# Optimization experiments

Measured on AMD Instinct MI355X. Metric: run time of the kernel, lower is better.

The kernel has to match this reference:

```python
import jax, jax.numpy as jnp
import numpy as np

B, T, D, H = 8, 512, 1024, 16
DK = D // H  # 64
EPS = 1e-3  # Keras BatchNormalization default epsilon


def batchnorm(x, gamma, beta):
    # Keras BN over feature axis (-1), training-mode batch statistics over (B, T)
    mean = jnp.mean(x, axis=(0, 1), keepdims=True)
    var = jnp.var(x, axis=(0, 1), keepdims=True)
    return (x - mean) * jax.lax.rsqrt(var + EPS) * gamma + beta


def setup_inputs() -> dict:
    key = jax.random.key(0)
    ks = jax.random.split(key, 12)
    s = 0.05
    return {
        "x": jax.random.normal(ks[0], (B, T, D), dtype=jnp.float32),
        "Wq": jax.random.uniform(ks[1], (H, D, DK), dtype=jnp.float32, minval=-s, maxval=s),
        "Wk": jax.random.uniform(ks[2], (H, D, DK), dtype=jnp.float32, minval=-s, maxval=s),
        "Wv": jax.random.uniform(ks[3], (H, D, DK), dtype=jnp.float32, minval=-s, maxval=s),
        "W": jax.random.uniform(ks[4], (D, D), dtype=jnp.float32, minval=-s, maxval=s),
        "W1": jax.random.normal(ks[5], (D, D), dtype=jnp.float32) * 0.02,
        "b1": jnp.zeros((D,), dtype=jnp.float32),
        "W2": jax.random.normal(ks[6], (D, D), dtype=jnp.float32) * 0.02,
        "b2": jnp.zeros((D,), dtype=jnp.float32),
        "g1": jnp.ones((D,), dtype=jnp.float32),
        "be1": jnp.zeros((D,), dtype=jnp.float32),
        "g2": jnp.ones((D,), dtype=jnp.float32),
        "be2": jnp.zeros((D,), dtype=jnp.float32),
    }


def reference(x, Wq, Wk, Wv, W, W1, b1, W2, b2, g1, be1, g2, be2):
    # Batched multi-head attention (replaces the per-head Python loop)
    q = jnp.einsum("btd,hdk->bhtk", x, Wq)
    k = jnp.einsum("btd,hdk->bhtk", x, Wk)
    v = jnp.einsum("btd,hdk->bhtk", x, Wv)
    scores = jnp.einsum("bhtk,bhsk->bhts", q, k) / jnp.sqrt(jnp.float32(DK))
    w = jax.nn.softmax(scores, axis=-1)
    attn = jnp.einsum("bhts,bhsk->bhtk", w, v)
    # concat heads: [B,H,T,DK] -> [B,T,H*DK] (head-major concat order as in the loop)
    concat = jnp.transpose(attn, (0, 2, 1, 3)).reshape(B, T, D)
    out = concat @ W
    out1 = batchnorm(x + out, g1, be1)
    out2 = jax.nn.relu(out1 @ W1 + b1) @ W2 + b2
    return batchnorm(out1 + out2, g2, be2)
```

## Files before the change

kernel.cpp:

```cpp
#include <hip/hip_runtime.h>
#include <hip/hip_bf16.h>
#include <cstdint>

#define Bn 8
#define Tn 512
#define Dn 1024
#define Hn 16
#define DKn 64
#define Mn (Bn * Tn)

typedef unsigned short u16;
typedef short bf16x8 __attribute__((ext_vector_type(8)));
typedef float f32x4 __attribute__((ext_vector_type(4)));

__device__ __forceinline__ u16 f2bf(float f) {
  unsigned int u = __builtin_bit_cast(unsigned int, f);
  u += 0x7fffu + ((u >> 16) & 1u);
  return (u16)(u >> 16);
}
__device__ __forceinline__ float bf2f(u16 v) {
  return __builtin_bit_cast(float, (unsigned int)v << 16);
}
__device__ __forceinline__ unsigned int pack2bf(float lo, float hi) {
  return (unsigned int)f2bf(lo) | ((unsigned int)f2bf(hi) << 16);
}

__device__ __forceinline__ void gl2lds16(const void* g, void* l) {
  __builtin_amdgcn_global_load_lds(
      (const __attribute__((address_space(1))) unsigned int*)g,
      (__attribute__((address_space(3))) unsigned int*)l,
      16, 0, 0);
}

__device__ __forceinline__ void bar() {
  asm volatile("" ::: "memory");
  __builtin_amdgcn_s_barrier();
  asm volatile("" ::: "memory");
}
#define WAITV(n_) asm volatile("s_waitcnt vmcnt(" #n_ ")" ::: "memory")

__global__ __launch_bounds__(256) void prep_k(
    const float* __restrict__ x, u16* __restrict__ xb,
    const float* __restrict__ wq, const float* __restrict__ wk,
    const float* __restrict__ wv, u16* __restrict__ wqkvT,
    const float* __restrict__ W, const float* __restrict__ W1,
    const float* __restrict__ W2, u16* __restrict__ wt,
    u16* __restrict__ w1t, u16* __restrict__ w2t)
{
  const int bid = blockIdx.x;
  const int t = threadIdx.x;
  if (bid < 2048) {
    const size_t i = ((size_t)bid * 256 + t) * 8;
    float4 a = *reinterpret_cast<const float4*>(&x[i]);
    float4 b = *reinterpret_cast<const float4*>(&x[i + 4]);
    uint4 w;
    w.x = pack2bf(a.x, a.y); w.y = pack2bf(a.z, a.w);
    w.z = pack2bf(b.x, b.y); w.w = pack2bf(b.z, b.w);
    *reinterpret_cast<uint4*>(&xb[i]) = w;
  } else if (bid < 2816) {
    const int idx = bid - 2048;
    const int kt = idx & 15;
    const int y  = idx >> 4;
    const int tau = y >> 4, head = y & 15;
    const float* src = (tau == 0 ? wq : tau == 1 ? wk : wv) + (size_t)head * 65536;
    const int n  = t & 63;
    const int kq = (t >> 6) << 4;
    const int k0 = kt << 6;
    u16 v[16];
#pragma unroll
    for (int j = 0; j < 16; j++)
      v[j] = f2bf(src[(size_t)(k0 + kq + j) * 64 + n]);
    u16* d = &wqkvT[((size_t)tau * 1024 + head * 64 + n) * 1024 + k0 + kq];
    *reinterpret_cast<uint4*>(&d[0]) = *reinterpret_cast<uint4*>(&v[0]);
    *reinterpret_cast<uint4*>(&d[8]) = *reinterpret_cast<uint4*>(&v[8]);
  } else {
    const int idx = bid - 2816;
    const int kt = idx & 15;
    const int rest = idx >> 4;
    const int ntl = rest & 15, z = rest >> 4;
    const float* src = (z == 0 ? W : z == 1 ? W1 : W2);
    u16* dst = (z == 0 ? wt : z == 1 ? w1t : w2t);
    const int n  = (ntl << 6) + (t & 63);
    const int kq = (t >> 6) << 4;
    const int k0 = kt << 6;
    u16 v[16];
#pragma unroll
    for (int j = 0; j < 16; j++)
      v[j] = f2bf(src[(size_t)(k0 + kq + j) * 1024 + n]);
    u16* d = &dst[(size_t)n * 1024 + k0 + kq];
    *reinterpret_cast<uint4*>(&d[0]) = *reinterpret_cast<uint4*>(&v[0]);
    *reinterpret_cast<uint4*>(&d[8]) = *reinterpret_cast<uint4*>(&v[8]);
  }
}

template<int VT>
__global__ __launch_bounds__(512) void mgemm_k(
    const u16* __restrict__ A, const u16* __restrict__ Bt,
    u16* __restrict__ Cb, int ldc, u16* __restrict__ Vt)
{
  __shared__ __align__(16) u16 As[3][4096];
  __shared__ __align__(16) u16 Bs[3][4096];

  const int nwg = gridDim.x * gridDim.y;
  const int fid = blockIdx.y * gridDim.x + blockIdx.x;
  const int lid = (fid & 7) * (nwg >> 3) + (fid >> 3);
  const int bx = lid % gridDim.x, by = lid / gridDim.x;

  const int tid  = threadIdx.x;
  const int lane = tid & 63;
  const int wid  = tid >> 6;
  const int wm = wid >> 2, wn = wid & 3;
  const int g4 = lane >> 4, r15 = lane & 15;
  const int m0 = by << 7, n0 = bx << 7;

  const int srow  = tid >> 2;
  const int sslot = tid & 3;
  const int ssw   = (srow ^ (srow >> 2)) & 3;
  const int sk8   = ((sslot ^ ssw) << 3);
  const u16* ga0 = &A[(size_t)(m0 + srow) * 1024 + sk8];
  const u16* gb0 = &Bt[(size_t)(n0 + srow) * 1024 + sk8];
  const int lofs = wid * 1024;

  f32x4 acc[4][2] = {};

  auto stage_t = [&](int t, int buf) {
    gl2lds16(ga0 + t * 32, (char*)As[buf] + lofs);
    gl2lds16(gb0 + t * 32, (char*)Bs[buf] + lofs);
  };
  auto compute_t = [&](int buf) {
    bf16x8 af[4], bfr[2];
#pragma unroll
    for (int m = 0; m < 4; m++) {
      int row = wm * 64 + m * 16 + r15;
      int sw = (row ^ (row >> 2)) & 3;
      af[m] = *reinterpret_cast<const bf16x8*>(
          (const char*)As[buf] + row * 64 + ((g4 ^ sw) << 4));
    }
#pragma unroll
    for (int n = 0; n < 2; n++) {
      int row = wn * 32 + n * 16 + r15;
      int sw = (row ^ (row >> 2)) & 3;
      bfr[n] = *reinterpret_cast<const bf16x8*>(
          (const char*)Bs[buf] + row * 64 + ((g4 ^ sw) << 4));
    }
#pragma unroll
    for (int m = 0; m < 4; m++)
#pragma unroll
      for (int n = 0; n < 2; n++)
        acc[m][n] = __builtin_amdgcn_mfma_f32_16x16x32_bf16(af[m], bfr[n], acc[m][n], 0, 0, 0);
  };

  stage_t(0, 0);
  stage_t(1, 1);

  int rd = 0, wr = 2;
#pragma unroll 1
  for (int t = 0; t < 30; ++t) {
    stage_t(t + 2, wr);
    WAITV(4);
    bar();
    compute_t(rd);
    bar();
    wr = rd;
    rd = (rd + 1 == 3) ? 0 : rd + 1;
  }
  WAITV(2);
  bar();
  compute_t(0);
  bar();
  WAITV(0);
  bar();
  compute_t(1);

  if (VT && bx >= 16) {
    const int vcol0 = n0 - 2048;
#pragma unroll
    for (int m = 0; m < 4; m++) {
      int row0 = m0 + wm * 64 + m * 16 + g4 * 4;
      int bI = row0 >> 9, s = row0 & 511;
#pragma unroll
      for (int n = 0; n < 2; n++) {
        int cv = vcol0 + wn * 32 + n * 16 + r15;
        int hh = cv >> 6, dk = cv & 63;
        uint2 pk;
        pk.x = pack2bf(acc[m][n][0], acc[m][n][1]);
        pk.y = pack2bf(acc[m][n][2], acc[m][n][3]);
        *reinterpret_cast<uint2*>(
            &Vt[(((size_t)(bI * 16 + hh) * 64 + dk) << 9) + s]) = pk;
      }
    }
    return;
  }

#pragma unroll
  for (int m = 0; m < 4; m++) {
    int row = m0 + wm * 64 + m * 16 + g4 * 4;
#pragma unroll
    for (int n = 0; n < 2; n++) {
      int col = n0 + wn * 32 + n * 16 + r15;
#pragma unroll
      for (int j = 0; j < 4; j++)
        Cb[(size_t)(row + j) * ldc + col] = f2bf(acc[m][n][j]);
    }
  }
}

template<int BIAS, int RELU, int OUTM, int RES, int RESNORM>
__global__ __launch_bounds__(512) void mgemm64_k(
    const u16* __restrict__ A, const u16* __restrict__ Bt,
    const float* __restrict__ bias, u16* __restrict__ Cb,
    const float* __restrict__ RresF, const u16* __restrict__ RresB,
    u16* __restrict__ Rout,
    float* __restrict__ psum, float* __restrict__ psumsq,
    const float* __restrict__ nsc, const float* __restrict__ nsh)
{
  __shared__ __align__(16) u16 As[3][2048];
  __shared__ __align__(16) u16 Bs[3][4096];

  const int nwg = gridDim.x * gridDim.y;
  const int fid = blockIdx.y * gridDim.x + blockIdx.x;
  const int lid = (fid & 7) * (nwg >> 3) + (fid >> 3);
  const int bx = lid % gridDim.x, by = lid / gridDim.x;

  const int tid  = threadIdx.x;
  const int lane = tid & 63;
  const int wid  = tid >> 6;
  const int wm = wid >> 2, wn = wid & 3;
  const int g4 = lane >> 4, r15 = lane & 15;
  const int m0 = by << 6, n0 = bx << 7;

  const int srow  = lane >> 2;
  const int sslot = lane & 3;
  const int arow  = (wid & 3) * 16 + srow;
  const int asw   = (arow ^ (arow >> 2)) & 3;
  const u16* gaP  = &A[(size_t)(m0 + arow) * 1024 + ((sslot ^ asw) << 3)];
  const int brow  = wid * 16 + srow;
  const int bsw   = (brow ^ (brow >> 2)) & 3;
  const u16* gbP  = &Bt[(size_t)(n0 + brow) * 1024 + ((sslot ^ bsw) << 3)];

  f32x4 acc[2][2] = {};

  auto stage_t = [&](int t, int buf) {
    if (wid < 4)
      gl2lds16(gaP + t * 32, (char*)As[buf] + (wid & 3) * 1024);
    gl2lds16(gbP + t * 32, (char*)Bs[buf] + wid * 1024);
  };
  auto compute_t = [&](int buf) {
    bf16x8 af[2], bfr[2];
#pragma unroll
    for (int m = 0; m < 2; m++) {
      int row = wm * 32 + m * 16 + r15;
      int sw = (row ^ (row >> 2)) & 3;
      af[m] = *reinterpret_cast<const bf16x8*>(
          (const char*)As[buf] + row * 64 + ((g4 ^ sw) << 4));
    }
#pragma unroll
    for (int n = 0; n < 2; n++) {
      int row = wn * 32 + n * 16 + r15;
      int sw = (row ^ (row >> 2)) & 3;
      bfr[n] = *reinterpret_cast<const bf16x8*>(
          (const char*)Bs[buf] + row * 64 + ((g4 ^ sw) << 4));
    }
#pragma unroll
    for (int m = 0; m < 2; m++)
#pragma unroll
      for (int n = 0; n < 2; n++)
        acc[m][n] = __builtin_amdgcn_mfma_f32_16x16x32_bf16(af[m], bfr[n], acc[m][n], 0, 0, 0);
  };

  stage_t(0, 0);
  stage_t(1, 1);

  int rd = 0, wr = 2;
#pragma unroll 1
  for (int t = 0; t < 30; ++t) {
    stage_t(t + 2, wr);
    if (wid < 4) { WAITV(4); } else { WAITV(2); }
    bar();
    compute_t(rd);
    bar();
    wr = rd;
    rd = (rd + 1 == 3) ? 0 : rd + 1;
  }
  if (wid < 4) { WAITV(2); } else { WAITV(1); }
  bar();
  compute_t(0);
  bar();
  WAITV(0);
  bar();
  compute_t(1);

  float bb[2] = {0.f, 0.f};
  if (BIAS) {
#pragma unroll
    for (int n = 0; n < 2; n++) bb[n] = bias[n0 + wn * 32 + n * 16 + r15];
  }

  if (RES) {
    float sc_[2], sh_[2];
    if (RESNORM) {
#pragma unroll
      for (int n = 0; n < 2; n++) {
        int col = n0 + wn * 32 + n * 16 + r15;
        sc_[n] = nsc[col];
        sh_[n] = nsh[col];
      }
    }
    float sp[2] = {0.f, 0.f}, sq[2] = {0.f, 0.f};
#pragma unroll
    for (int m = 0; m < 2; m++) {
      int row = m0 + wm * 32 + m * 16 + g4 * 4;
#pragma unroll
      for (int n = 0; n < 2; n++) {
        int col = n0 + wn * 32 + n * 16 + r15;
#pragma unroll
        for (int j = 0; j < 4; j++) {
          size_t off = (size_t)(row + j) * 1024 + col;
          float v = acc[m][n][j] + bb[n];
          float res;
          if (RESNORM) res = fmaf(bf2f(RresB[off]), sc_[n], sh_[n]);
          else         res = RresF[off];
          float r = v + res;
          Rout[off] = f2bf(r);
          sp[n] += r;
          sq[n] = fmaf(r, r, sq[n]);
        }
      }
    }
#pragma unroll
    for (int n = 0; n < 2; n++) {
      sp[n] += __shfl_xor(sp[n], 16, 64);
      sp[n] += __shfl_xor(sp[n], 32, 64);
      sq[n] += __shfl_xor(sq[n], 16, 64);
      sq[n] += __shfl_xor(sq[n], 32, 64);
    }
    if (g4 == 0) {
      int slot = (by << 1) + wm;
#pragma unroll
      for (int n = 0; n < 2; n++) {
        int col = n0 + wn * 32 + n * 16 + r15;
        psum[(size_t)slot * 1024 + col] = sp[n];
        psumsq[(size_t)slot * 1024 + col] = sq[n];
      }
    }
    return;
  }

#pragma unroll
  for (int m = 0; m < 2; m++) {
    int row = m0 + wm * 32 + m * 16 + g4 * 4;
#pragma unroll
    for (int n = 0; n < 2; n++) {
      int col = n0 + wn * 32 + n * 16 + r15;
#pragma unroll
      for (int j = 0; j < 4; j++) {
        float v = acc[m][n][j];
        if (BIAS) v += bb[n];
        if (RELU) v = fmaxf(v, 0.f);
        if (OUTM == 1) Cb[(size_t)(row + j) * 1024 + col] = f2bf(v);
      }
    }
  }
}

__global__ __launch_bounds__(256, 2) void attn_k(
    const u16* __restrict__ qk, const u16* __restrict__ Vt,
    u16* __restrict__ o)
{
  __shared__ __align__(16) unsigned char Ks[2][16384];
  __shared__ __align__(16) unsigned char Vs[2][16384];
  __shared__ __align__(16) unsigned char Ps[16384];

  const int bh  = blockIdx.x;
  const int qc  = blockIdx.y;
  const int b   = bh >> 4, h = bh & 15;
  const int tid = threadIdx.x;
  const int lane = tid & 63;
  const int wv   = tid >> 6;
  const int qcol = lane & 15;
  const int g    = lane >> 4;

  const size_t rowbase = (size_t)b * Tn;
  const size_t qrow0   = rowbase + qc * 64 + wv * 16;

  bf16x8 qf[2];
  {
    const u16* qp = &qk[(qrow0 + qcol) * 2048 + h * 64 + g * 8];
    qf[0] = *reinterpret_cast<const bf16x8*>(qp);
    qf[1] = *reinterpret_cast<const bf16x8*>(qp + 32);
  }

  f32x4 oa[4] = {};
  float m_run = -3e38f, l_run = 0.f;

  const int krow = tid >> 3, kch = tid & 7;
  const int vrow = tid >> 4, vch = tid & 15;
  unsigned char* Pw = &Ps[wv * 4096];

  auto stage_kv = [&](int c, int buf) {
#pragma unroll
    for (int i = 0; i < 4; i++) {
      int row = i * 32 + krow;
      const u16* gk = &qk[(rowbase + c * 128 + row) * 2048 + 1024 + h * 64
                          + ((kch ^ (row & 7)) << 3)];
      gl2lds16(gk, (char*)Ks[buf] + wv * 1024 + i * 4096);
    }
#pragma unroll
    for (int i = 0; i < 4; i++) {
      int row = i * 16 + vrow;
      const u16* gv = &Vt[(((size_t)bh * 64 + row) << 9) + c * 128
                          + ((vch ^ (row & 7)) << 3)];
      gl2lds16(gv, (char*)Vs[buf] + wv * 1024 + i * 4096);
    }
  };

  auto compute_c = [&](int cur) {
    f32x4 sf[8];
#pragma unroll
    for (int t = 0; t < 8; t++) {
      sf[t] = (f32x4){0.f, 0.f, 0.f, 0.f};
      const int srow = t * 16 + qcol;
      const int base = srow * 128;
      const int sw = srow & 7;
#pragma unroll
      for (int ks = 0; ks < 2; ks++) {
        bf16x8 a = *reinterpret_cast<const bf16x8*>(
            &Ks[cur][base + (((ks * 4 + g) ^ sw) << 4)]);
        sf[t] = __builtin_amdgcn_mfma_f32_16x16x32_bf16(a, qf[ks], sf[t], 0, 0, 0);
      }
    }

    float mc = -3e38f;
#pragma unroll
    for (int t = 0; t < 8; t++)
#pragma unroll
      for (int r = 0; r < 4; r++) {
        float s = sf[t][r] * 0.125f;
        sf[t][r] = s;
        mc = fmaxf(mc, s);
      }
    mc = fmaxf(mc, __shfl_xor(mc, 16, 64));
    mc = fmaxf(mc, __shfl_xor(mc, 32, 64));
    float mnew = fmaxf(m_run, mc);
    float alpha = __expf(m_run - mnew);
    m_run = mnew;

    float lsum = 0.f;
#pragma unroll
    for (int t = 0; t < 8; t++)
#pragma unroll
      for (int r = 0; r < 4; r++) {
        float e = __expf(sf[t][r] - mnew);
        sf[t][r] = e;
        lsum += e;
      }
    lsum += __shfl_xor(lsum, 16, 64);
    lsum += __shfl_xor(lsum, 32, 64);
    l_run = l_run * alpha + lsum;

#pragma unroll
    for (int j = 0; j < 4; j++) {
      float av = __shfl(alpha, (g << 4) + g * 4 + j, 64);
#pragma unroll
      for (int nt = 0; nt < 4; nt++) oa[nt][j] *= av;
    }

#pragma unroll
    for (int t = 0; t < 8; t++) {
      int o0 = t * 32 + g * 8;
      int chunk = o0 >> 4;
      int sb = ((chunk ^ (qcol & 7)) << 4) | (o0 & 15);
      *reinterpret_cast<unsigned int*>(&Pw[qcol * 256 + sb]) =
          pack2bf(sf[t][0], sf[t][1]);
      *reinterpret_cast<unsigned int*>(&Pw[qcol * 256 + sb + 4]) =
          pack2bf(sf[t][2], sf[t][3]);
    }

    bf16x8 pa[4];
#pragma unroll
    for (int ks = 0; ks < 4; ks++)
      pa[ks] = *reinterpret_cast<const bf16x8*>(
          &Pw[qcol * 256 + (((ks * 4 + g) ^ (qcol & 7)) << 4)]);
#pragma unroll
    for (int nt = 0; nt < 4; nt++) {
      const int vr = nt * 16 + qcol;
      const int vsw = vr & 7;
#pragma unroll
      for (int ks = 0; ks < 4; ks++) {
        bf16x8 bvf = *reinterpret_cast<const bf16x8*>(
            &Vs[cur][vr * 256 + (((ks * 4 + g) ^ vsw) << 4)]);
        oa[nt] = __builtin_amdgcn_mfma_f32_16x16x32_bf16(pa[ks], bvf, oa[nt], 0, 0, 0);
      }
    }
  };

  stage_kv(0, 0);
#pragma unroll 1
  for (int c = 0; c < 3; ++c) {
    stage_kv(c + 1, (c + 1) & 1);
    WAITV(8);
    bar();
    compute_c(c & 1);
    bar();
  }
  WAITV(0);
  bar();
  compute_c(1);

  float rl = 1.f / l_run;
#pragma unroll
  for (int j = 0; j < 4; j++) {
    float il = __shfl(rl, (g << 4) + g * 4 + j, 64);
#pragma unroll
    for (int nt = 0; nt < 4; nt++)
      o[(qrow0 + g * 4 + j) * 1024 + h * 64 + nt * 16 + qcol] =
          f2bf(oa[nt][j] * il);
  }
}

__global__ __launch_bounds__(256) void reduce_stats_k(
    const float* __restrict__ ps, const float* __restrict__ pq,
    const float* __restrict__ g, const float* __restrict__ be,
    float* __restrict__ scale, float* __restrict__ shift)
{
  const int col = blockIdx.x * 256 + threadIdx.x;
  float s = 0.f, q = 0.f;
  for (int p = 0; p < 128; p++) {
    s += ps[(size_t)p * Dn + col];
    q += pq[(size_t)p * Dn + col];
  }
  const float invn = 1.f / 4096.f;
  float mean = s * invn;
  float var = q * invn - mean * mean;
  float inv = rsqrtf(var + 1e-3f);
  float sc = g[col] * inv;
  scale[col] = sc;
  shift[col] = be[col] - mean * sc;
}

template<int OUTMODE>
__global__ __launch_bounds__(256) void norm_k(
    const u16* __restrict__ r, const float* __restrict__ scale,
    const float* __restrict__ shift, float* __restrict__ o, u16* __restrict__ ob)
{
  const size_t i8 = ((size_t)blockIdx.x * 256 + threadIdx.x) * 8;
  const int col = (int)(i8 & 1023);
  uint4 rv = *reinterpret_cast<const uint4*>(&r[i8]);
  const u16* rs = reinterpret_cast<const u16*>(&rv);
  float4 sc0 = *reinterpret_cast<const float4*>(&scale[col]);
  float4 sc1 = *reinterpret_cast<const float4*>(&scale[col + 4]);
  float4 sh0 = *reinterpret_cast<const float4*>(&shift[col]);
  float4 sh1 = *reinterpret_cast<const float4*>(&shift[col + 4]);
  const float scs[8] = {sc0.x, sc0.y, sc0.z, sc0.w, sc1.x, sc1.y, sc1.z, sc1.w};
  const float shs[8] = {sh0.x, sh0.y, sh0.z, sh0.w, sh1.x, sh1.y, sh1.z, sh1.w};
  float v[8];
#pragma unroll
  for (int j = 0; j < 8; j++)
    v[j] = fmaf(bf2f(rs[j]), scs[j], shs[j]);
  if (OUTMODE == 0) {
    float4 o0 = make_float4(v[0], v[1], v[2], v[3]);
    float4 o1 = make_float4(v[4], v[5], v[6], v[7]);
    *reinterpret_cast<float4*>(&o[i8]) = o0;
    *reinterpret_cast<float4*>(&o[i8 + 4]) = o1;
  } else {
    uint4 p;
    p.x = pack2bf(v[0], v[1]); p.y = pack2bf(v[2], v[3]);
    p.z = pack2bf(v[4], v[5]); p.w = pack2bf(v[6], v[7]);
    *reinterpret_cast<uint4*>(&ob[i8]) = p;
  }
}

extern "C" void kernel_launch(void* const* d_in, const int* in_sizes, int n_in,
                              void* d_out, int out_size, void* d_ws, size_t ws_size,
                              hipStream_t stream)
{
  const float* x   = (const float*)d_in[0];
  const float* wq  = (const float*)d_in[1];
  const float* wk  = (const float*)d_in[2];
  const float* wv  = (const float*)d_in[3];
  const float* W   = (const float*)d_in[4];
  const float* W1  = (const float*)d_in[5];
  const float* b1  = (const float*)d_in[6];
  const float* W2  = (const float*)d_in[7];
  const float* b2  = (const float*)d_in[8];
  const float* g1  = (const float*)d_in[9];
  const float* be1 = (const float*)d_in[10];
  const float* g2  = (const float*)d_in[11];
  const float* be2 = (const float*)d_in[12];

  float* out = (float*)d_out;
  float* ws  = (float*)d_ws;

  const size_t NB = (size_t)Mn * Dn;
  float* psum   = ws;
  float* psumsq = psum + 128 * Dn;
  float* scale1 = psumsq + 128 * Dn;
  float* shift1 = scale1 + Dn;
  float* scale2 = shift1 + Dn;
  float* shift2 = scale2 + Dn;
  u16* ws1b    = (u16*)(shift2 + Dn);
  u16* ws2b    = ws1b + NB;
  u16* xb      = ws2b + NB;
  u16* qkb     = xb + NB;
  u16* vtb     = qkb + 2 * NB;
  u16* concatb = vtb + NB;
  u16* wqkvT   = concatb + NB;
  u16* wt      = wqkvT + 3 * 1048576;
  u16* w1t     = wt + 1048576;
  u16* w2t     = w1t + 1048576;
  u16* out1b = qkb;
  u16* hb    = qkb + NB;

  dim3 b256(256), b512(512);

  prep_k<<<dim3(3584), b256, 0, stream>>>(x, xb, wq, wk, wv, wqkvT,
                                          W, W1, W2, wt, w1t, w2t);
  mgemm_k<1><<<dim3(24, 32), b512, 0, stream>>>(xb, wqkvT, qkb, 2048, vtb);
  attn_k<<<dim3(128, 8), b256, 0, stream>>>(qkb, vtb, concatb);
  mgemm64_k<0, 0, 2, 1, 0><<<dim3(8, 64), b512, 0, stream>>>(
      concatb, wt, nullptr, nullptr, x, nullptr, ws1b, psum, psumsq,
      nullptr, nullptr);
  reduce_stats_k<<<dim3(4), b256, 0, stream>>>(psum, psumsq, g1, be1, scale1, shift1);
  norm_k<2><<<dim3(2048), b256, 0, stream>>>(ws1b, scale1, shift1, nullptr, out1b);
  mgemm64_k<1, 1, 1, 0, 0><<<dim3(8, 64), b512, 0, stream>>>(
      out1b, w1t, b1, hb, nullptr, nullptr, nullptr, nullptr, nullptr,
      nullptr, nullptr);
  mgemm64_k<1, 0, 2, 1, 1><<<dim3(8, 64), b512, 0, stream>>>(
      hb, w2t, b2, nullptr, nullptr, ws1b, ws2b, psum, psumsq,
      scale1, shift1);
  reduce_stats_k<<<dim3(4), b256, 0, stream>>>(psum, psumsq, g2, be2, scale2, shift2);
  norm_k<0><<<dim3(2048), b256, 0, stream>>>(ws2b, scale2, shift2, out, nullptr);
}
```

Before: 171.4 us.

## Stage V transpose in LDS, lazy softmax rescale, parallel stats reduce, bf16 residual

The V-transpose epilogue of the QKV GEMM is staged through shared memory so each thread writes contiguous 64-byte runs of Vt instead of scattered 8-byte stores. The attention kernel raises wave priority around its MFMA blocks and skips the running-max update and output rescale when the new chunk max exceeds the running max by at most 8. The BN stats reduction is spread over 32 blocks, each combining partials through shared memory. The first residual now reads bf16 x instead of fp32 x, halving that read but adding a rounding step on the residual.

```diff
diff --git a/kernel.cpp b/kernel.cpp
--- a/kernel.cpp
+++ b/kernel.cpp
@@ -173,21 +173,39 @@
   compute_t(1);
 
   if (VT && bx >= 16) {
+    bar();
     const int vcol0 = n0 - 2048;
 #pragma unroll
     for (int m = 0; m < 4; m++) {
-      int row0 = m0 + wm * 64 + m * 16 + g4 * 4;
-      int bI = row0 >> 9, s = row0 & 511;
+      int sloc = wm * 64 + m * 16 + g4 * 4;
 #pragma unroll
       for (int n = 0; n < 2; n++) {
-        int cv = vcol0 + wn * 32 + n * 16 + r15;
-        int hh = cv >> 6, dk = cv & 63;
+        int cv = wn * 32 + n * 16 + r15;
+        u16* base = (cv < 64) ? (u16*)As : (u16*)Bs;
         uint2 pk;
         pk.x = pack2bf(acc[m][n][0], acc[m][n][1]);
         pk.y = pack2bf(acc[m][n][2], acc[m][n][3]);
-        *reinterpret_cast<uint2*>(
-            &Vt[(((size_t)(bI * 16 + hh) * 64 + dk) << 9) + s]) = pk;
-      }
+        *reinterpret_cast<uint2*>(&base[(size_t)(cv & 63) * 136 + sloc]) = pk;
+      }
+    }
+    bar();
+    {
+      int cv = tid >> 2;
+      int sch = (tid & 3) << 5;
+      const u16* base = (cv < 64) ? (const u16*)As : (const u16*)Bs;
+      const u16* src = &base[(size_t)(cv & 63) * 136 + sch];
+      uint4 v0 = *reinterpret_cast<const uint4*>(src);
+      uint4 v1 = *reinterpret_cast<const uint4*>(src + 8);
+      uint4 v2 = *reinterpret_cast<const uint4*>(src + 16);
+      uint4 v3 = *reinterpret_cast<const uint4*>(src + 24);
+      int vcol = vcol0 + cv;
+      int hh = vcol >> 6, dk = vcol & 63;
+      int bI = m0 >> 9, sbase = (m0 & 511) + sch;
+      u16* dst = &Vt[(((size_t)(bI * 16 + hh) * 64 + dk) << 9) + sbase];
+      *reinterpret_cast<uint4*>(dst) = v0;
+      *reinterpret_cast<uint4*>(dst + 8) = v1;
+      *reinterpret_cast<uint4*>(dst + 16) = v2;
+      *reinterpret_cast<uint4*>(dst + 24) = v3;
     }
     return;
   }
@@ -209,8 +227,7 @@
 __global__ __launch_bounds__(512) void mgemm64_k(
     const u16* __restrict__ A, const u16* __restrict__ Bt,
     const float* __restrict__ bias, u16* __restrict__ Cb,
-    const float* __restrict__ RresF, const u16* __restrict__ RresB,
-    u16* __restrict__ Rout,
+    const u16* __restrict__ RresB, u16* __restrict__ Rout,
     float* __restrict__ psum, float* __restrict__ psumsq,
     const float* __restrict__ nsc, const float* __restrict__ nsh)
 {
@@ -317,9 +334,8 @@
         for (int j = 0; j < 4; j++) {
           size_t off = (size_t)(row + j) * 1024 + col;
           float v = acc[m][n][j] + bb[n];
-          float res;
-          if (RESNORM) res = fmaf(bf2f(RresB[off]), sc_[n], sh_[n]);
-          else         res = RresF[off];
+          float res = bf2f(RresB[off]);
+          if (RESNORM) res = fmaf(res, sc_[n], sh_[n]);
           float r = v + res;
           Rout[off] = f2bf(r);
           sp[n] += r;
@@ -416,6 +432,7 @@
 
   auto compute_c = [&](int cur) {
     f32x4 sf[8];
+    __builtin_amdgcn_s_setprio(1);
 #pragma unroll
     for (int t = 0; t < 8; t++) {
       sf[t] = (f32x4){0.f, 0.f, 0.f, 0.f};
@@ -429,6 +446,7 @@
         sf[t] = __builtin_amdgcn_mfma_f32_16x16x32_bf16(a, qf[ks], sf[t], 0, 0, 0);
       }
     }
+    __builtin_amdgcn_s_setprio(0);
 
     float mc = -3e38f;
 #pragma unroll
@@ -441,28 +459,42 @@
       }
     mc = fmaxf(mc, __shfl_xor(mc, 16, 64));
     mc = fmaxf(mc, __shfl_xor(mc, 32, 64));
-    float mnew = fmaxf(m_run, mc);
-    float alpha = __expf(m_run - mnew);
-    m_run = mnew;
-
-    float lsum = 0.f;
-#pragma unroll
-    for (int t = 0; t < 8; t++)
-#pragma unroll
-      for (int r = 0; r < 4; r++) {
-        float e = __expf(sf[t][r] - mnew);
-        sf[t][r] = e;
-        lsum += e;
-      }
-    lsum += __shfl_xor(lsum, 16, 64);
-    lsum += __shfl_xor(lsum, 32, 64);
-    l_run = l_run * alpha + lsum;
-
-#pragma unroll
-    for (int j = 0; j < 4; j++) {
-      float av = __shfl(alpha, (g << 4) + g * 4 + j, 64);
-#pragma unroll
-      for (int nt = 0; nt < 4; nt++) oa[nt][j] *= av;
+
+    if (__all(mc - m_run <= 8.f)) {
+      float lsum = 0.f;
+#pragma unroll
+      for (int t = 0; t < 8; t++)
+#pragma unroll
+        for (int r = 0; r < 4; r++) {
+          float e = __expf(sf[t][r] - m_run);
+          sf[t][r] = e;
+          lsum += e;
+        }
+      lsum += __shfl_xor(lsum, 16, 64);
+      lsum += __shfl_xor(lsum, 32, 64);
+      l_run += lsum;
+    } else {
+      float mnew = fmaxf(m_run, mc);
+      float alpha = __expf(m_run - mnew);
+      m_run = mnew;
+      float lsum = 0.f;
+#pragma unroll
+      for (int t = 0; t < 8; t++)
+#pragma unroll
+        for (int r = 0; r < 4; r++) {
+          float e = __expf(sf[t][r] - mnew);
+          sf[t][r] = e;
+          lsum += e;
+        }
+      lsum += __shfl_xor(lsum, 16, 64);
+      lsum += __shfl_xor(lsum, 32, 64);
+      l_run = l_run * alpha + lsum;
+#pragma unroll
+      for (int j = 0; j < 4; j++) {
+        float av = __shfl(alpha, (g << 4) + g * 4 + j, 64);
+#pragma unroll
+        for (int nt = 0; nt < 4; nt++) oa[nt][j] *= av;
+      }
     }
 
 #pragma unroll
@@ -481,6 +513,7 @@
     for (int ks = 0; ks < 4; ks++)
       pa[ks] = *reinterpret_cast<const bf16x8*>(
           &Pw[qcol * 256 + (((ks * 4 + g) ^ (qcol & 7)) << 4)]);
+    __builtin_amdgcn_s_setprio(1);
 #pragma unroll
     for (int nt = 0; nt < 4; nt++) {
       const int vr = nt * 16 + qcol;
@@ -492,6 +525,7 @@
         oa[nt] = __builtin_amdgcn_mfma_f32_16x16x32_bf16(pa[ks], bvf, oa[nt], 0, 0, 0);
       }
     }
+    __builtin_amdgcn_s_setprio(0);
   };
 
   stage_kv(0, 0);
@@ -523,19 +557,32 @@
     const float* __restrict__ g, const float* __restrict__ be,
     float* __restrict__ scale, float* __restrict__ shift)
 {
-  const int col = blockIdx.x * 256 + threadIdx.x;
+  __shared__ float Ls[8][32], Lq[8][32];
+  const int t = threadIdx.x;
+  const int col = blockIdx.x * 32 + (t & 31);
+  const int rg = t >> 5;
   float s = 0.f, q = 0.f;
-  for (int p = 0; p < 128; p++) {
+#pragma unroll
+  for (int i = 0; i < 16; i++) {
+    int p = rg * 16 + i;
     s += ps[(size_t)p * Dn + col];
     q += pq[(size_t)p * Dn + col];
   }
-  const float invn = 1.f / 4096.f;
-  float mean = s * invn;
-  float var = q * invn - mean * mean;
-  float inv = rsqrtf(var + 1e-3f);
-  float sc = g[col] * inv;
-  scale[col] = sc;
-  shift[col] = be[col] - mean * sc;
+  Ls[rg][t & 31] = s;
+  Lq[rg][t & 31] = q;
+  __syncthreads();
+  if (t < 32) {
+    float S = 0.f, Q = 0.f;
+#pragma unroll
+    for (int r = 0; r < 8; r++) { S += Ls[r][t]; Q += Lq[r][t]; }
+    const float invn = 1.f / 4096.f;
+    float mean = S * invn;
+    float var = Q * invn - mean * mean;
+    float inv = rsqrtf(var + 1e-3f);
+    float sc = g[col] * inv;
+    scale[col] = sc;
+    shift[col] = be[col] - mean * sc;
+  }
 }
 
 template<int OUTMODE>
@@ -618,16 +665,16 @@
   mgemm_k<1><<<dim3(24, 32), b512, 0, stream>>>(xb, wqkvT, qkb, 2048, vtb);
   attn_k<<<dim3(128, 8), b256, 0, stream>>>(qkb, vtb, concatb);
   mgemm64_k<0, 0, 2, 1, 0><<<dim3(8, 64), b512, 0, stream>>>(
-      concatb, wt, nullptr, nullptr, x, nullptr, ws1b, psum, psumsq,
+      concatb, wt, nullptr, nullptr, xb, ws1b, psum, psumsq,
       nullptr, nullptr);
-  reduce_stats_k<<<dim3(4), b256, 0, stream>>>(psum, psumsq, g1, be1, scale1, shift1);
+  reduce_stats_k<<<dim3(32), b256, 0, stream>>>(psum, psumsq, g1, be1, scale1, shift1);
   norm_k<2><<<dim3(2048), b256, 0, stream>>>(ws1b, scale1, shift1, nullptr, out1b);
   mgemm64_k<1, 1, 1, 0, 0><<<dim3(8, 64), b512, 0, stream>>>(
-      out1b, w1t, b1, hb, nullptr, nullptr, nullptr, nullptr, nullptr,
+      out1b, w1t, b1, hb, nullptr, nullptr, nullptr, nullptr,
       nullptr, nullptr);
   mgemm64_k<1, 0, 2, 1, 1><<<dim3(8, 64), b512, 0, stream>>>(
-      hb, w2t, b2, nullptr, nullptr, ws1b, ws2b, psum, psumsq,
+      hb, w2t, b2, nullptr, ws1b, ws2b, psum, psumsq,
       scale1, shift1);
-  reduce_stats_k<<<dim3(4), b256, 0, stream>>>(psum, psumsq, g2, be2, scale2, shift2);
+  reduce_stats_k<<<dim3(32), b256, 0, stream>>>(psum, psumsq, g2, be2, scale2, shift2);
   norm_k<0><<<dim3(2048), b256, 0, stream>>>(ws2b, scale2, shift2, out, nullptr);
 }
```

Measured after the change: 144.8 us. 15.5% less time.
